# Optimization experiments

Hardware: AMD Instinct MI355X
Metric: run time of the kernel (lower is better)

The kernel has to match this reference:

```python
import jax, jax.numpy as jnp
import numpy as np
import math

N = 4096          # nodes
E = 131072        # edges (avg degree 32)
H = 128           # hidden_channels
IN = 128          # in_channels
RATIO = 0.8
K = int(math.ceil(RATIO * N))   # clusters kept by ASAPooling (static)


def setup_inputs():
    key = jax.random.key(0)
    ks = jax.random.split(key, 24)
    sc = 0.05
    def p(i, shape):
        return jax.random.normal(ks[i], shape, dtype=jnp.float32) * sc
    x = jax.random.normal(ks[0], (N, IN), dtype=jnp.float32)
    src = jax.random.randint(ks[1], (E,), 0, N)
    off = jax.random.randint(ks[2], (E,), 0, N - 1)
    dst = (src + 1 + off) % N          # guaranteed no self-loops
    edge_index = jnp.stack([src, dst]).astype(jnp.int32)
    inp = {"x": x, "edge_index": edge_index}
    dims = [(IN, H), (H, H), (H, H), (H, H)]
    for ci, (din, dout) in enumerate(dims):
        inp[f"c{ci}_Wrel"] = p(3 + 3 * ci, (dout, din))
        inp[f"c{ci}_brel"] = jnp.zeros((dout,), jnp.float32)
        inp[f"c{ci}_Wroot"] = p(4 + 3 * ci, (dout, din))
    inp["p_Wlin"] = p(16, (H, H));     inp["p_blin"] = jnp.zeros((H,), jnp.float32)
    inp["p_Watt"] = p(17, (1, 2 * H)); inp["p_batt"] = jnp.zeros((1,), jnp.float32)
    inp["p_W1"] = p(18, (1, H));       inp["p_b1"] = jnp.zeros((1,), jnp.float32)
    inp["p_W2"] = p(19, (1, H))
    inp["p_W3"] = p(20, (1, H));       inp["p_b3"] = jnp.zeros((1,), jnp.float32)
    return inp


def _graph_conv_edges(x, src, dst, Wrel, brel, Wroot):
    # GraphConv(aggr='mean'), edge_weight=None: lin_rel(mean_j x_j) + lin_root(x)
    n = x.shape[0]
    agg = jax.ops.segment_sum(x[src], dst, num_segments=n)
    deg = jax.ops.segment_sum(jnp.ones((src.shape[0],), x.dtype), dst, num_segments=n)
    mean = agg / jnp.maximum(deg, 1.0)[:, None]
    return mean @ Wrel.T + brel + x @ Wroot.T


def _graph_conv_dense(x, A, Wrel, brel, Wroot):
    # A[j, i] = weight of edge j -> i; mean over existing (nonzero) edges
    agg = jnp.einsum('ji,jh->ih', A, x)
    deg = (A != 0).astype(x.dtype).sum(axis=0)
    mean = agg / jnp.maximum(deg, 1.0)[:, None]
    return mean @ Wrel.T + brel + x @ Wroot.T


def _asap_pool(x, src, dst, Wlin, blin, Watt, batt, W1, b1, W2, W3, b3):
    n = x.shape[0]
    loops = jnp.arange(n, dtype=src.dtype)
    s2 = jnp.concatenate([src, loops])           # add_remaining_self_loops (w=1)
    d2 = jnp.concatenate([dst, loops])
    x_pool_j = x[s2]                              # [E2, H]
    x_q = jax.ops.segment_max(x_pool_j, d2, num_segments=n)   # cluster max
    x_q = (x_q @ Wlin.T + blin)[d2]
    score = jnp.concatenate([x_q, x_pool_j], axis=-1) @ Watt.T + batt
    score = jax.nn.leaky_relu(score[:, 0], 0.2)
    m = jax.ops.segment_max(score, d2, num_segments=n)        # stable edge softmax
    ex = jnp.exp(score - m[d2])
    score = ex / jax.ops.segment_sum(ex, d2, num_segments=n)[d2]
    x_new = jax.ops.segment_sum(x[s2] * score[:, None], d2, num_segments=n)
    # fitness via LEConv(H -> 1) with all edge weights 1
    a = x_new @ W1.T + b1
    b = x_new @ W2.T
    agg = jax.ops.segment_sum(a[s2] - b[d2], d2, num_segments=n)
    fitness = jax.nn.sigmoid(agg + x_new @ W3.T + b3)[:, 0]
    fit_k, perm = jax.lax.top_k(fitness, K)
    xp = x_new[perm] * fit_k[:, None]
    # graph coarsening: A' = S^T A S, S restricted to kept clusters
    S = jnp.zeros((n, n), x.dtype).at[s2, d2].add(score)[:, perm]   # [n, K]
    A = jnp.zeros((n, n), x.dtype).at[s2, d2].add(1.0)
    A2 = S.T @ (A @ S)
    A2 = A2 * (1.0 - jnp.eye(K, dtype=x.dtype))  # remove_diag (add_self_loops=False)
    return xp, A2


def _forward(x, edge_index, c0_Wrel, c0_brel, c0_Wroot, c1_Wrel, c1_brel, c1_Wroot,
             c2_Wrel, c2_brel, c2_Wroot, c3_Wrel, c3_brel, c3_Wroot,
             p_Wlin, p_blin, p_Watt, p_batt, p_W1, p_b1, p_W2, p_W3, p_b3):
    src, dst = edge_index[0], edge_index[1]
    x1 = jax.nn.relu(_graph_conv_edges(x, src, dst, c0_Wrel, c0_brel, c0_Wroot))
    xs = [x1.mean(axis=0, keepdims=True)]                 # global_mean_pool, B=1
    x2 = jax.nn.relu(_graph_conv_edges(x1, src, dst, c1_Wrel, c1_brel, c1_Wroot))
    xs.append(x2.mean(axis=0, keepdims=True))
    xp, A = _asap_pool(x2, src, dst, p_Wlin, p_blin, p_Watt, p_batt,
                       p_W1, p_b1, p_W2, p_W3, p_b3)
    x3 = jax.nn.relu(_graph_conv_dense(xp, A, c2_Wrel, c2_brel, c2_Wroot))
    xs.append(x3.mean(axis=0, keepdims=True))
    x4 = jax.nn.relu(_graph_conv_dense(x3, A, c3_Wrel, c3_brel, c3_Wroot))
    xs.append(x4.mean(axis=0, keepdims=True))
    return jnp.concatenate(xs, axis=1)    # JumpingKnowledge 'cat': [1, 4*H]


def reference(x, edge_index, c0_Wrel, c0_brel, c0_Wroot, c1_Wrel, c1_brel, c1_Wroot,
              c2_Wrel, c2_brel, c2_Wroot, c3_Wrel, c3_brel, c3_Wroot,
              p_Wlin, p_blin, p_Watt, p_batt, p_W1, p_b1, p_W2, p_W3, p_b3):
    return _forward(x, edge_index, c0_Wrel, c0_brel, c0_Wroot, c1_Wrel, c1_brel,
                    c1_Wroot, c2_Wrel, c2_brel, c2_Wroot, c3_Wrel, c3_brel, c3_Wroot,
                    p_Wlin, p_blin, p_Watt, p_batt, p_W1, p_b1, p_W2, p_W3, p_b3)
```

## Files before the change

kernel.cpp:

```cpp
#include <hip/hip_runtime.h>
#include <hip/hip_fp16.h>
#include <math.h>

namespace {

constexpr int NN = 4096;
constexpr int EE = 131072;
constexpr int E2 = EE + NN;
constexpr int HH = 128;
constexpr int KC = 3277;
constexpr int UPW = 104;
constexpr int WSB = (E2 + 255) / 256;
constexpr int XPB = (KC*HH + 255) / 256;

typedef _Float16 f16x8 __attribute__((ext_vector_type(8)));
typedef float f32x4 __attribute__((ext_vector_type(4)));

__device__ __forceinline__ float lrelu02(float x){ return x > 0.f ? x : 0.2f * x; }

__device__ __forceinline__ float redSum128(float* red, int t, float v){
  red[t] = v; __syncthreads();
  #pragma unroll
  for (int s = 64; s > 0; s >>= 1){ if (t < s) red[t] += red[t + s]; __syncthreads(); }
  float r = red[0]; __syncthreads();
  return r;
}
__device__ __forceinline__ float redMax128(float* red, int t, float v){
  red[t] = v; __syncthreads();
  #pragma unroll
  for (int s = 64; s > 0; s >>= 1){ if (t < s) red[t] = fmaxf(red[t], red[t + s]); __syncthreads(); }
  float r = red[0]; __syncthreads();
  return r;
}

__global__ void k_count(const int* __restrict__ ei, int* cntD, int* cntS){
  int e = blockIdx.x * blockDim.x + threadIdx.x;
  if (e >= E2) return;
  int u, v;
  if (e < EE){ u = ei[e]; v = ei[EE + e]; } else { u = e - EE; v = u; }
  atomicAdd(&cntD[v], 1);
  atomicAdd(&cntS[u], 1);
}

__global__ void k_scan(const int* cntD, const int* cntS, int* rowD, int* rowS, int* curD, int* curS){
  __shared__ unsigned long long wsum[16];
  int t = threadIdx.x, lane = t & 63, wid = t >> 6;
  int d0 = cntD[t*4], d1 = cntD[t*4+1], d2 = cntD[t*4+2], d3 = cntD[t*4+3];
  int s0 = cntS[t*4], s1 = cntS[t*4+1], s2 = cntS[t*4+2], s3 = cntS[t*4+3];
  int dT = d0 + d1 + d2 + d3, sT = s0 + s1 + s2 + s3;
  unsigned long long tot = ((unsigned long long)(unsigned)dT << 32) | (unsigned)sT;
  unsigned long long x = tot;
  #pragma unroll
  for (int offs = 1; offs < 64; offs <<= 1){
    unsigned long long v = __shfl_up(x, offs);
    if (lane >= offs) x += v;
  }
  if (lane == 63) wsum[wid] = x;
  __syncthreads();
  if (t == 0){
    unsigned long long acc = 0;
    for (int i = 0; i < 16; ++i){ unsigned long long tmp = wsum[i]; wsum[i] = acc; acc += tmp; }
  }
  __syncthreads();
  unsigned long long excl = x - tot + wsum[wid];
  int eD = (int)(excl >> 32), eS = (int)(excl & 0xFFFFFFFFull);
  int r0 = eD, r1 = r0 + d0, r2 = r1 + d1, r3 = r2 + d2;
  rowD[t*4] = r0; rowD[t*4+1] = r1; rowD[t*4+2] = r2; rowD[t*4+3] = r3;
  curD[t*4] = r0; curD[t*4+1] = r1; curD[t*4+2] = r2; curD[t*4+3] = r3;
  int q0 = eS, q1 = q0 + s0, q2 = q1 + s1, q3 = q2 + s2;
  rowS[t*4] = q0; rowS[t*4+1] = q1; rowS[t*4+2] = q2; rowS[t*4+3] = q3;
  curS[t*4] = q0; curS[t*4+1] = q1; curS[t*4+2] = q2; curS[t*4+3] = q3;
  if (t == 1023){ rowD[NN] = r3 + d3; rowS[NN] = q3 + s3; }
}

__global__ void k_scatter(const int* __restrict__ ei, int* curD, int* curS,
                          int* colD, int* dstS, int* mapSD){
  int e = blockIdx.x * blockDim.x + threadIdx.x;
  if (e >= E2) return;
  int u, v;
  if (e < EE){ u = ei[e]; v = ei[EE + e]; } else { u = e - EE; v = u; }
  int p = atomicAdd(&curD[v], 1); colD[p] = u;
  int q = atomicAdd(&curS[u], 1); dstS[q] = v; mapSD[q] = p;
}

__global__ void k_prep(const float* __restrict__ x,
                       const float* __restrict__ W0rel, const float* __restrict__ W0root,
                       const float* __restrict__ W1rel, const float* __restrict__ W1root,
                       const float* __restrict__ W2rel, const float* __restrict__ W2root,
                       const float* __restrict__ W3rel, const float* __restrict__ W3root,
                       const float* __restrict__ Wlin, const float* __restrict__ blin,
                       const float* __restrict__ Watt,
                       __half* __restrict__ xh, __half* __restrict__ WH, float* __restrict__ wA2,
                       int* cntD, int* cntS, float* out){
  int b = blockIdx.x;
  if (b < 2048){
    int i = b*256 + threadIdx.x;
    xh[i] = __float2half(x[i]);
  } else if (b < 2048 + 512){
    int i = (b - 2048)*256 + threadIdx.x;
    int m = i >> 14, o = i & 16383;
    const float* src;
    switch (m){
      case 0: src = W0rel; break;
      case 1: src = W0root; break;
      case 2: src = W1rel; break;
      case 3: src = W1root; break;
      case 4: src = W2rel; break;
      case 5: src = W2root; break;
      case 6: src = W3rel; break;
      default: src = W3root; break;
    }
    WH[i] = __float2half(src[o]);
  } else if (b == 2560){
    int c = threadIdx.x;
    if (c < 128){
      float s = 0.f;
      for (int hh = 0; hh < HH; ++hh) s += Watt[hh] * Wlin[hh*HH + c];
      wA2[c] = s;
      if (c == 0){
        float q = 0.f;
        for (int hh = 0; hh < HH; ++hh) q += blin[hh] * Watt[hh];
        wA2[HH] = q;
      }
    }
  } else {
    int i = (b - 2561)*256 + threadIdx.x;
    cntD[i] = 0; cntS[i] = 0;
    if (i < 512) out[i] = 0.f;
  }
}

__global__ void k_edge_meanH(const __half* __restrict__ xinh, const int* __restrict__ rowD,
                             const int* __restrict__ colD, __half* __restrict__ meanbh){
  int v = blockIdx.x, t = threadIdx.x;
  int beg = rowD[v], end = rowD[v+1];
  float acc = 0.f;
  int p = beg;
  for (; p + 8 <= end; p += 8){
    int u0 = colD[p],   u1 = colD[p+1], u2 = colD[p+2], u3 = colD[p+3];
    int u4 = colD[p+4], u5 = colD[p+5], u6 = colD[p+6], u7 = colD[p+7];
    float a0 = __half2float(xinh[(size_t)u0*HH + t]);
    float a1 = __half2float(xinh[(size_t)u1*HH + t]);
    float a2 = __half2float(xinh[(size_t)u2*HH + t]);
    float a3 = __half2float(xinh[(size_t)u3*HH + t]);
    float a4 = __half2float(xinh[(size_t)u4*HH + t]);
    float a5 = __half2float(xinh[(size_t)u5*HH + t]);
    float a6 = __half2float(xinh[(size_t)u6*HH + t]);
    float a7 = __half2float(xinh[(size_t)u7*HH + t]);
    if (u0 != v) acc += a0;
    if (u1 != v) acc += a1;
    if (u2 != v) acc += a2;
    if (u3 != v) acc += a3;
    if (u4 != v) acc += a4;
    if (u5 != v) acc += a5;
    if (u6 != v) acc += a6;
    if (u7 != v) acc += a7;
  }
  for (; p < end; ++p){ int u = colD[p]; if (u != v) acc += __half2float(xinh[(size_t)u*HH + t]); }
  float dg = (float)(end - beg - 1);
  meanbh[(size_t)v*HH + t] = __float2half(acc / fmaxf(dg, 1.f));
}

__global__ void k_linM(const __half* __restrict__ mh, const __half* __restrict__ xinh,
                       const __half* __restrict__ WHh, int woff, int rows,
                       const float* __restrict__ brel,
                       float* __restrict__ xout, __half* __restrict__ xouth,
                       float* __restrict__ cmout,
                       const float* __restrict__ WattFull, float* __restrict__ xdotp){
  __shared__ float sx[16][4];
  int t = threadIdx.x, lane = t & 63, w = t >> 6;
  int r0 = blockIdx.x * 16;
  int l15 = lane & 15, lk = (lane >> 4) * 8;
  const _Float16* WH = (const _Float16*)WHh;
  const _Float16* Am = (const _Float16*)mh + (size_t)(r0 + l15)*HH + lk;
  const _Float16* Ax = (const _Float16*)xinh + (size_t)(r0 + l15)*HH + lk;
  const _Float16* Brel0 = WH + woff + (size_t)(w*32 + l15)*HH + lk;
  const _Float16* Brel1 = Brel0 + (size_t)16*HH;
  const _Float16* Broot0 = Brel0 + 16384;
  const _Float16* Broot1 = Brel1 + 16384;
  f32x4 acc0 = (f32x4)0.f, acc1 = (f32x4)0.f;
  #pragma unroll
  for (int kk = 0; kk < HH; kk += 32){
    f16x8 a = *(const f16x8*)(Am + kk);
    f16x8 b0 = *(const f16x8*)(Brel0 + kk);
    f16x8 b1 = *(const f16x8*)(Brel1 + kk);
    acc0 = __builtin_amdgcn_mfma_f32_16x16x32_f16(a, b0, acc0, 0, 0, 0);
    acc1 = __builtin_amdgcn_mfma_f32_16x16x32_f16(a, b1, acc1, 0, 0, 0);
  }
  #pragma unroll
  for (int kk = 0; kk < HH; kk += 32){
    f16x8 a = *(const f16x8*)(Ax + kk);
    f16x8 b0 = *(const f16x8*)(Broot0 + kk);
    f16x8 b1 = *(const f16x8*)(Broot1 + kk);
    acc0 = __builtin_amdgcn_mfma_f32_16x16x32_f16(a, b0, acc0, 0, 0, 0);
    acc1 = __builtin_amdgcn_mfma_f32_16x16x32_f16(a, b1, acc1, 0, 0, 0);
  }
  int rbase = (lane >> 4) * 4;
  int h0 = w*32 + l15, h1 = h0 + 16;
  float bb0 = brel[h0], bb1 = brel[h1];
  float wt0 = 0.f, wt1 = 0.f;
  if (xdotp){ wt0 = WattFull[HH + h0]; wt1 = WattFull[HH + h1]; }
  float cs0 = 0.f, cs1 = 0.f;
  #pragma unroll
  for (int r = 0; r < 4; ++r){
    int row = r0 + rbase + r;
    float v0 = fmaxf(acc0[r] + bb0, 0.f);
    float v1 = fmaxf(acc1[r] + bb1, 0.f);
    if (row < rows){
      if (xout){ xout[(size_t)row*HH + h0] = v0; xout[(size_t)row*HH + h1] = v1; }
      if (xouth){ xouth[(size_t)row*HH + h0] = __float2half(v0); xouth[(size_t)row*HH + h1] = __float2half(v1); }
      cs0 += v0; cs1 += v1;
    }
    if (xdotp){
      float ds = (row < rows) ? (v0*wt0 + v1*wt1) : 0.f;
      ds += __shfl_xor(ds, 1); ds += __shfl_xor(ds, 2);
      ds += __shfl_xor(ds, 4); ds += __shfl_xor(ds, 8);
      if (l15 == 0) sx[rbase + r][w] = ds;
    }
  }
  cs0 += __shfl_xor(cs0, 16); cs0 += __shfl_xor(cs0, 32);
  cs1 += __shfl_xor(cs1, 16); cs1 += __shfl_xor(cs1, 32);
  if (lane < 16){
    atomicAdd(&cmout[h0], cs0 / (float)rows);
    atomicAdd(&cmout[h1], cs1 / (float)rows);
  }
  if (xdotp){
    __syncthreads();
    if (t < 16 && r0 + t < rows) xdotp[r0 + t] = sx[t][0] + sx[t][1] + sx[t][2] + sx[t][3];
  }
}

__global__ void k_pool(const __half* __restrict__ x2h, const int* __restrict__ rowD, const int* __restrict__ colD,
                       const float* __restrict__ xdotA, const float* __restrict__ wA2, const float* __restrict__ battp,
                       const float* __restrict__ W1, const float* __restrict__ b1,
                       const float* __restrict__ W2, const float* __restrict__ W3, const float* __restrict__ b3,
                       float* qdotA, float* mA, float* sA, float* __restrict__ xnew, float* __restrict__ wD,
                       float* aA, float* bA, float* cA, float* __restrict__ diag2){
  __shared__ float red[128];
  __shared__ float wmem[128];
  __shared__ int uc[128];
  __shared__ int srcL[1024];
  __shared__ float wL[1024];
  int v = blockIdx.x, t = threadIdx.x;
  int beg = rowD[v], end = rowD[v+1];
  float batt = battp[0];
  float mx = -3.402823466e38f;
  int p = beg;
  for (; p + 4 <= end; p += 4){
    float a0 = __half2float(x2h[(size_t)colD[p]*HH + t]);
    float a1 = __half2float(x2h[(size_t)colD[p+1]*HH + t]);
    float a2 = __half2float(x2h[(size_t)colD[p+2]*HH + t]);
    float a3 = __half2float(x2h[(size_t)colD[p+3]*HH + t]);
    mx = fmaxf(fmaxf(fmaxf(fmaxf(mx, a0), a1), a2), a3);
  }
  for (; p < end; ++p) mx = fmaxf(mx, __half2float(x2h[(size_t)colD[p]*HH + t]));
  float qd = redSum128(red, t, mx * wA2[t]) + wA2[HH];
  float lm = -3.402823466e38f;
  for (p = beg + t; p < end; p += 128) lm = fmaxf(lm, lrelu02(qd + xdotA[colD[p]] + batt));
  float mm = redMax128(red, t, lm);
  float ls = 0.f;
  for (p = beg + t; p < end; p += 128) ls += expf(lrelu02(qd + xdotA[colD[p]] + batt) - mm);
  float ss = redSum128(red, t, ls);
  float acc = 0.f;
  for (int basep = beg; basep < end; basep += 128){
    int cnt = min(128, end - basep);
    if (t < cnt){
      int u = colD[basep + t];
      uc[t] = u;
      float w = expf(lrelu02(qd + xdotA[u] + batt) - mm) / ss;
      wmem[t] = w;
      wD[basep + t] = w;
      int o = basep - beg + t;
      if (o < 1024){ srcL[o] = u; wL[o] = w; }
    }
    __syncthreads();
    int i = 0;
    for (; i + 4 <= cnt; i += 4){
      float a0 = __half2float(x2h[(size_t)uc[i]*HH + t]);
      float a1 = __half2float(x2h[(size_t)uc[i+1]*HH + t]);
      float a2 = __half2float(x2h[(size_t)uc[i+2]*HH + t]);
      float a3 = __half2float(x2h[(size_t)uc[i+3]*HH + t]);
      acc += wmem[i]*a0 + wmem[i+1]*a1 + wmem[i+2]*a2 + wmem[i+3]*a3;
    }
    for (; i < cnt; ++i) acc += wmem[i] * __half2float(x2h[(size_t)uc[i]*HH + t]);
    __syncthreads();
  }
  xnew[(size_t)v*HH + t] = acc;
  float s1 = redSum128(red, t, acc * W1[t]);
  float s2 = redSum128(red, t, acc * W2[t]);
  float s3 = redSum128(red, t, acc * W3[t]);
  int d = end - beg; if (d > 1024) d = 1024;
  float dpart = 0.f;
  for (int pp = t; pp < d; pp += 128){
    int s = srcL[pp];
    float sp = 0.f;
    for (int q = 0; q < d; ++q) if (srcL[q] == s) sp += wL[q];
    dpart += wL[pp] * sp;
  }
  float d2 = redSum128(red, t, dpart);
  if (t == 0){
    qdotA[v] = qd; mA[v] = mm; sA[v] = ss;
    aA[v] = s1 + b1[0]; bA[v] = s2; cA[v] = s3 + b3[0];
    diag2[v] = d2;
  }
}

__global__ void k_fit(const int* __restrict__ rowD, const int* __restrict__ colD,
                      const float* __restrict__ aA, const float* __restrict__ bA, const float* __restrict__ cA,
                      float* __restrict__ fitA){
  __shared__ float red[128];
  int v = blockIdx.x, t = threadIdx.x;
  int beg = rowD[v], end = rowD[v+1];
  float la = 0.f;
  for (int p = beg + t; p < end; p += 128) la += aA[colD[p]];
  float s = redSum128(red, t, la);
  if (t == 0){
    float g = s - (float)(end - beg) * bA[v] + cA[v];
    fitA[v] = 1.f / (1.f + expf(-g));
  }
}

__global__ void k_sel(const float* __restrict__ fitA, int* perm, float* fitk, int* kcol){
  __shared__ unsigned keys[NN];
  __shared__ int hist[256];
  __shared__ int sufA[257];
  __shared__ int wsum[16];
  __shared__ int bc[2];
  int t = threadIdx.x, lane = t & 63, wid = t >> 6;
  #pragma unroll
  for (int r = 0; r < 4; ++r){
    int i = t + r*1024;
    unsigned b = __float_as_uint(fitA[i]);
    keys[i] = (b & 0x80000000u) ? ~b : (b ^ 0x80000000u);
  }
  __syncthreads();
  unsigned prefix = 0;
  int kneed = KC;
  #pragma unroll
  for (int round = 0; round < 4; ++round){
    int shift = 24 - round*8;
    unsigned pmask = (round == 0) ? 0u : (0xFFFFFFFFu << (shift + 8));
    if (t < 256) hist[t] = 0;
    __syncthreads();
    #pragma unroll
    for (int r = 0; r < 4; ++r){
      unsigned kv = keys[t + r*1024];
      if ((kv & pmask) == prefix)
        atomicAdd(&hist[(kv >> shift) & 0xFF], 1);
    }
    __syncthreads();
    int x = (t < 256) ? hist[t] : 0;
    #pragma unroll
    for (int offs = 1; offs < 64; offs <<= 1){
      int v = __shfl_down(x, offs);
      if (lane + offs < 64) x += v;
    }
    if (t < 256 && lane == 0) wsum[wid] = x;
    if (t == 0) sufA[256] = 0;
    __syncthreads();
    if (t < 256){
      int add = 0;
      #pragma unroll
      for (int w2 = 1; w2 < 4; ++w2) if (wid + w2 < 4) add += wsum[wid + w2];
      sufA[t] = x + add;
    }
    __syncthreads();
    if (t < 256){
      if (sufA[t] >= kneed && sufA[t+1] < kneed){ bc[0] = t; bc[1] = kneed - sufA[t+1]; }
    }
    __syncthreads();
    prefix |= ((unsigned)bc[0]) << shift;
    kneed = bc[1];
    __syncthreads();
  }
  unsigned T = prefix;
  int need_eq = kneed;
  int cnt[4]; int tot = 0;
  #pragma unroll
  for (int r = 0; r < 4; ++r){
    unsigned kv = keys[t*4 + r];
    int g = (kv > T) ? 1 : 0;
    int e = (kv == T) ? 1 : 0;
    cnt[r] = (g << 16) | e;
    tot += cnt[r];
  }
  int x2 = tot;
  #pragma unroll
  for (int offs = 1; offs < 64; offs <<= 1){
    int v = __shfl_up(x2, offs);
    if (lane >= offs) x2 += v;
  }
  if (lane == 63) wsum[wid] = x2;
  __syncthreads();
  if (t < 16){
    int y = wsum[t];
    #pragma unroll
    for (int offs = 1; offs < 16; offs <<= 1){
      int v = __shfl_up(y, offs);
      if (t >= offs) y += v;
    }
    wsum[t] = y;
  }
  __syncthreads();
  int waveoff = (wid > 0) ? wsum[wid - 1] : 0;
  int inc = x2 + waveoff;
  int run = inc - tot;
  int gtot = wsum[15] >> 16;
  #pragma unroll
  for (int r = 0; r < 4; ++r){
    int i = t*4 + r;
    int g = cnt[r] >> 16, e = cnt[r] & 0xFFFF;
    int gpos = run >> 16, epos = run & 0xFFFF;
    int pos = -1;
    if (g) pos = gpos;
    else if (e && epos < need_eq) pos = gtot + epos;
    if (pos >= 0){ perm[pos] = i; fitk[pos] = fitA[i]; kcol[i] = pos; }
    else kcol[i] = -1;
    run += cnt[r];
  }
}

__global__ void k_post(const int* __restrict__ mapSD, const int* __restrict__ dstS,
                       const int* __restrict__ kcol, const float* __restrict__ wD,
                       int2* __restrict__ kwS,
                       const float* __restrict__ xnew, const int* __restrict__ perm,
                       const float* __restrict__ fitk, __half* __restrict__ xph){
  int b = blockIdx.x;
  if (b < WSB){
    int q = b*256 + threadIdx.x;
    if (q >= E2) return;
    float w = wD[mapSD[q]];
    int k = kcol[dstS[q]];
    kwS[q] = make_int2(k, __float_as_int(w));
  } else {
    int idx = (b - WSB)*256 + threadIdx.x;
    if (idx >= KC*HH) return;
    int j = idx >> 7;
    float v = xnew[(size_t)perm[j]*HH + (idx & 127)] * fitk[j];
    xph[idx] = __float2half(v);
  }
}

__global__ void k_y1(const int* __restrict__ rowS, const int2* __restrict__ kwS,
                     const __half* __restrict__ Xh, __half* __restrict__ Y1h,
                     unsigned* __restrict__ UP, int emitUP){
  __shared__ int kArr[128];
  __shared__ float wArr[128];
  __shared__ unsigned upw[UPW];
  int n = blockIdx.x, t = threadIdx.x;
  if (emitUP && t < UPW) upw[t] = 0u;
  int beg = rowS[n], end = rowS[n+1];
  float acc = 0.f;
  for (int basep = beg; basep < end; basep += 128){
    int cnt = min(128, end - basep);
    if (t < cnt){
      int2 kw = kwS[basep + t];
      kArr[t] = kw.x;
      wArr[t] = __int_as_float(kw.y);
      if (emitUP && kw.x >= 0) atomicOr(&upw[kw.x >> 5], 1u << (kw.x & 31));
    }
    __syncthreads();
    for (int i = 0; i < cnt; ++i){
      int k = kArr[i];
      if (k >= 0) acc += wArr[i] * __half2float(Xh[(size_t)k*HH + t]);
    }
    __syncthreads();
  }
  Y1h[(size_t)n*HH + t] = __float2half(acc);
  if (emitUP){
    __syncthreads();
    if (t < UPW) UP[(size_t)n*UPW + t] = upw[t];
  }
}

__global__ void k_y2p(const int* __restrict__ rowD, const int* __restrict__ colD,
                      const __half* __restrict__ Y1h, __half* __restrict__ Y2h,
                      const int* __restrict__ perm, const unsigned* __restrict__ UP,
                      unsigned* __restrict__ PAT){
  int b = blockIdx.x, t = threadIdx.x;
  if (b < NN){
    int m = b;
    int beg = rowD[m], end = rowD[m+1];
    float acc = 0.f;
    int p = beg;
    for (; p + 8 <= end; p += 8){
      float a0 = __half2float(Y1h[(size_t)colD[p]*HH + t]);
      float a1 = __half2float(Y1h[(size_t)colD[p+1]*HH + t]);
      float a2 = __half2float(Y1h[(size_t)colD[p+2]*HH + t]);
      float a3 = __half2float(Y1h[(size_t)colD[p+3]*HH + t]);
      float a4 = __half2float(Y1h[(size_t)colD[p+4]*HH + t]);
      float a5 = __half2float(Y1h[(size_t)colD[p+5]*HH + t]);
      float a6 = __half2float(Y1h[(size_t)colD[p+6]*HH + t]);
      float a7 = __half2float(Y1h[(size_t)colD[p+7]*HH + t]);
      acc += ((a0 + a1) + (a2 + a3)) + ((a4 + a5) + (a6 + a7));
    }
    for (; p < end; ++p) acc += __half2float(Y1h[(size_t)colD[p]*HH + t]);
    Y2h[(size_t)m*HH + t] = __float2half(acc);
  } else {
    int k1 = b - NN;
    if (k1 >= KC || t >= UPW) return;
    int v = perm[k1];
    int beg = rowD[v], end = rowD[v+1];
    unsigned pw = 0u;
    for (int p = beg; p < end; ++p) pw |= UP[(size_t)colD[p]*UPW + t];
    PAT[(size_t)k1*UPW + t] = pw;
  }
}

__global__ void k_y2(const int* __restrict__ rowD, const int* __restrict__ colD,
                     const __half* __restrict__ Y1h, __half* __restrict__ Y2h){
  int m = blockIdx.x, t = threadIdx.x;
  int beg = rowD[m], end = rowD[m+1];
  float acc = 0.f;
  int p = beg;
  for (; p + 8 <= end; p += 8){
    float a0 = __half2float(Y1h[(size_t)colD[p]*HH + t]);
    float a1 = __half2float(Y1h[(size_t)colD[p+1]*HH + t]);
    float a2 = __half2float(Y1h[(size_t)colD[p+2]*HH + t]);
    float a3 = __half2float(Y1h[(size_t)colD[p+3]*HH + t]);
    float a4 = __half2float(Y1h[(size_t)colD[p+4]*HH + t]);
    float a5 = __half2float(Y1h[(size_t)colD[p+5]*HH + t]);
    float a6 = __half2float(Y1h[(size_t)colD[p+6]*HH + t]);
    float a7 = __half2float(Y1h[(size_t)colD[p+7]*HH + t]);
    acc += ((a0 + a1) + (a2 + a3)) + ((a4 + a5) + (a6 + a7));
  }
  for (; p < end; ++p) acc += __half2float(Y1h[(size_t)colD[p]*HH + t]);
  Y2h[(size_t)m*HH + t] = __float2half(acc);
}

__global__ void k_z(const int* __restrict__ rowD, const int* __restrict__ colD,
                    const float* __restrict__ wD, const int* __restrict__ perm,
                    const __half* __restrict__ Y2h, const __half* __restrict__ Xh,
                    const float* __restrict__ diag2, const int* __restrict__ degN,
                    __half* __restrict__ meanbh){
  __shared__ int uc[128];
  __shared__ float wm[128];
  int k = blockIdx.x, t = threadIdx.x;
  int v = perm[k];
  int beg = rowD[v], end = rowD[v+1];
  float acc = 0.f;
  for (int basep = beg; basep < end; basep += 128){
    int cnt = min(128, end - basep);
    if (t < cnt){ uc[t] = colD[basep + t]; wm[t] = wD[basep + t]; }
    __syncthreads();
    int i = 0;
    for (; i + 4 <= cnt; i += 4){
      float a0 = __half2float(Y2h[(size_t)uc[i]*HH + t]);
      float a1 = __half2float(Y2h[(size_t)uc[i+1]*HH + t]);
      float a2 = __half2float(Y2h[(size_t)uc[i+2]*HH + t]);
      float a3 = __half2float(Y2h[(size_t)uc[i+3]*HH + t]);
      acc += wm[i]*a0 + wm[i+1]*a1 + wm[i+2]*a2 + wm[i+3]*a3;
    }
    for (; i < cnt; ++i) acc += wm[i] * __half2float(Y2h[(size_t)uc[i]*HH + t]);
    __syncthreads();
  }
  float d = fmaxf((float)degN[k], 1.f);
  float xv = __half2float(Xh[(size_t)k*HH + t]);
  meanbh[(size_t)k*HH + t] = __float2half((acc - diag2[v] * xv) / d);
}

__global__ void k_degc(const unsigned* __restrict__ PAT, int* __restrict__ degN){
  __shared__ int red[256];
  int w = blockIdx.x, t = threadIdx.x;
  int c[32];
  #pragma unroll
  for (int j = 0; j < 32; ++j) c[j] = 0;
  for (int r = t; r < KC; r += 256){
    unsigned b = PAT[(size_t)r*UPW + w];
    #pragma unroll
    for (int j = 0; j < 32; ++j) c[j] += (b >> j) & 1;
  }
  for (int j = 0; j < 32; ++j){
    red[t] = c[j]; __syncthreads();
    #pragma unroll
    for (int s = 128; s > 0; s >>= 1){ if (t < s) red[t] += red[t + s]; __syncthreads(); }
    if (t == 0) degN[w*32 + j] = red[0] - 1;
    __syncthreads();
  }
}

}

extern "C" void kernel_launch(void* const* d_in, const int* in_sizes, int n_in,
                              void* d_out, int out_size, void* d_ws, size_t ws_size,
                              hipStream_t stream){
  (void)in_sizes; (void)n_in; (void)out_size; (void)ws_size;
  const float* x      = (const float*)d_in[0];
  const int*   ei     = (const int*)d_in[1];
  const float* c0Wrel = (const float*)d_in[2];
  const float* c0brel = (const float*)d_in[3];
  const float* c0Wroot= (const float*)d_in[4];
  const float* c1Wrel = (const float*)d_in[5];
  const float* c1brel = (const float*)d_in[6];
  const float* c1Wroot= (const float*)d_in[7];
  const float* c2Wrel = (const float*)d_in[8];
  const float* c2brel = (const float*)d_in[9];
  const float* c2Wroot= (const float*)d_in[10];
  const float* c3Wrel = (const float*)d_in[11];
  const float* c3brel = (const float*)d_in[12];
  const float* c3Wroot= (const float*)d_in[13];
  const float* Wlin   = (const float*)d_in[14];
  const float* blin   = (const float*)d_in[15];
  const float* Watt   = (const float*)d_in[16];
  const float* batt   = (const float*)d_in[17];
  const float* W1     = (const float*)d_in[18];
  const float* b1     = (const float*)d_in[19];
  const float* W2     = (const float*)d_in[20];
  const float* W3     = (const float*)d_in[21];
  const float* b3     = (const float*)d_in[22];
  float* out = (float*)d_out;

  char* base = (char*)d_ws;
  size_t off = 0;
  auto carve = [&](size_t bytes) -> void* {
    void* p = base + off;
    off += (bytes + 255) & ~(size_t)255;
    return p;
  };
  float* xnew  = (float*)carve((size_t)NN*HH*4);
  __half* xh   = (__half*)carve((size_t)NN*HH*2);
  __half* x1h  = (__half*)carve((size_t)NN*HH*2);
  __half* x2bh = (__half*)carve((size_t)NN*HH*2);
  __half* mbh  = (__half*)carve((size_t)NN*HH*2);
  __half* xph  = (__half*)carve((size_t)(KC+16)*HH*2);
  __half* x3h  = (__half*)carve((size_t)(KC+16)*HH*2);
  __half* Y1h  = (__half*)carve((size_t)NN*HH*2);
  __half* Y2h  = (__half*)carve((size_t)NN*HH*2);
  __half* WH   = (__half*)carve((size_t)8*HH*HH*2);
  unsigned* UP  = (unsigned*)carve((size_t)NN*UPW*4);
  unsigned* PAT = (unsigned*)carve((size_t)KC*UPW*4);
  float* xdot  = (float*)carve(NN*4);
  float* qdot  = (float*)carve(NN*4);
  float* mmaxA = (float*)carve(NN*4);
  float* ssumA = (float*)carve(NN*4);
  float* aA    = (float*)carve(NN*4);
  float* bA    = (float*)carve(NN*4);
  float* cA    = (float*)carve(NN*4);
  float* fitA  = (float*)carve(NN*4);
  float* fitk  = (float*)carve(KC*4);
  float* wA2   = (float*)carve((HH+1)*4);
  float* wD    = (float*)carve((size_t)E2*4);
  float* diag2 = (float*)carve(NN*4);
  int* rowD = (int*)carve((NN+1)*4);
  int* rowS = (int*)carve((NN+1)*4);
  int* cntD = (int*)carve(NN*4);
  int* cntS = (int*)carve(NN*4);
  int* curD = (int*)carve(NN*4);
  int* curS = (int*)carve(NN*4);
  int* colD = (int*)carve((size_t)E2*4);
  int* dstS = (int*)carve((size_t)E2*4);
  int* mapSD= (int*)carve((size_t)E2*4);
  int2* kwS = (int2*)carve((size_t)E2*8);
  int* perm = (int*)carve(KC*4);
  int* kcol = (int*)carve(NN*4);
  int* degN = (int*)carve((size_t)UPW*32*4);

  k_prep<<<2048 + 512 + 1 + 16, 256, 0, stream>>>(x, c0Wrel, c0Wroot, c1Wrel, c1Wroot,
                                                  c2Wrel, c2Wroot, c3Wrel, c3Wroot,
                                                  Wlin, blin, Watt, xh, WH, wA2,
                                                  cntD, cntS, out);
  k_count<<<(E2+255)/256, 256, 0, stream>>>(ei, cntD, cntS);
  k_scan<<<1, 1024, 0, stream>>>(cntD, cntS, rowD, rowS, curD, curS);
  k_scatter<<<(E2+255)/256, 256, 0, stream>>>(ei, curD, curS, colD, dstS, mapSD);

  k_edge_meanH<<<NN, 128, 0, stream>>>(xh, rowD, colD, mbh);
  k_linM<<<NN/16, 256, 0, stream>>>(mbh, xh, WH, 0, NN, c0brel,
                                    nullptr, x1h, out + 0, nullptr, nullptr);

  k_edge_meanH<<<NN, 128, 0, stream>>>(x1h, rowD, colD, mbh);
  k_linM<<<NN/16, 256, 0, stream>>>(mbh, x1h, WH, 32768, NN, c1brel,
                                    nullptr, x2bh, out + 128, Watt, xdot);

  k_pool<<<NN, 128, 0, stream>>>(x2bh, rowD, colD, xdot, wA2, batt,
                                 W1, b1, W2, W3, b3,
                                 qdot, mmaxA, ssumA, xnew, wD, aA, bA, cA, diag2);
  k_fit<<<NN, 128, 0, stream>>>(rowD, colD, aA, bA, cA, fitA);
  k_sel<<<1, 1024, 0, stream>>>(fitA, perm, fitk, kcol);
  k_post<<<WSB + XPB, 256, 0, stream>>>(mapSD, dstS, kcol, wD, kwS,
                                        xnew, perm, fitk, xph);

  k_y1<<<NN, 128, 0, stream>>>(rowS, kwS, xph, Y1h, UP, 1);
  k_y2p<<<NN + KC, 128, 0, stream>>>(rowD, colD, Y1h, Y2h, perm, UP, PAT);
  k_degc<<<UPW, 256, 0, stream>>>(PAT, degN);
  k_z<<<KC, 128, 0, stream>>>(rowD, colD, wD, perm, Y2h, xph, diag2, degN, mbh);
  k_linM<<<(KC+15)/16, 256, 0, stream>>>(mbh, xph, WH, 65536, KC, c2brel,
                                         nullptr, x3h, out + 256, nullptr, nullptr);

  k_y1<<<NN, 128, 0, stream>>>(rowS, kwS, x3h, Y1h, UP, 0);
  k_y2<<<NN, 128, 0, stream>>>(rowD, colD, Y1h, Y2h);
  k_z<<<KC, 128, 0, stream>>>(rowD, colD, wD, perm, Y2h, x3h, diag2, degN, mbh);
  k_linM<<<(KC+15)/16, 256, 0, stream>>>(mbh, x3h, WH, 98304, KC, c3brel,
                                         nullptr, nullptr, out + 384, nullptr, nullptr);
}
```

Measured before the change: 240.3 us.

## Vectorize gather kernels with half2 loads and split edges across two waves

Rewrites the neighbour-gather kernels (edge mean, pool, Y1/Y2, z) so each thread loads a __half2 covering two channels instead of one half. The two 64-lane wavefronts of each 128-thread block take alternating edges, and their partial sums are combined through shared memory. The aim is to double bytes per load instruction and halve per-wave edge iterations in these latency-bound gathers. It adds a shared-memory reduction and barrier, and leaves half the threads idle during the final writes. In k_pool the 128-wide block reductions are replaced with wave shuffles.

Result: faster. 233.4 us (-2.9%).

```diff
diff --git a/kernel.cpp b/kernel.cpp
--- a/kernel.cpp
+++ b/kernel.cpp
@@ -31,6 +31,11 @@
   for (int s = 64; s > 0; s >>= 1){ if (t < s) red[t] = fmaxf(red[t], red[t + s]); __syncthreads(); }
   float r = red[0]; __syncthreads();
   return r;
+}
+__device__ __forceinline__ float waveRed64(float v){
+  #pragma unroll
+  for (int o = 32; o > 0; o >>= 1) v += __shfl_xor(v, o);
+  return v;
 }
 
 __global__ void k_count(const int* __restrict__ ei, int* cntD, int* cntS){
@@ -132,33 +137,35 @@
 
 __global__ void k_edge_meanH(const __half* __restrict__ xinh, const int* __restrict__ rowD,
                              const int* __restrict__ colD, __half* __restrict__ meanbh){
+  __shared__ float2 s2[128];
   int v = blockIdx.x, t = threadIdx.x;
+  int c = t & 63, g = t >> 6;
+  const __half2* X2 = (const __half2*)xinh;
   int beg = rowD[v], end = rowD[v+1];
-  float acc = 0.f;
-  int p = beg;
-  for (; p + 8 <= end; p += 8){
-    int u0 = colD[p],   u1 = colD[p+1], u2 = colD[p+2], u3 = colD[p+3];
-    int u4 = colD[p+4], u5 = colD[p+5], u6 = colD[p+6], u7 = colD[p+7];
-    float a0 = __half2float(xinh[(size_t)u0*HH + t]);
-    float a1 = __half2float(xinh[(size_t)u1*HH + t]);
-    float a2 = __half2float(xinh[(size_t)u2*HH + t]);
-    float a3 = __half2float(xinh[(size_t)u3*HH + t]);
-    float a4 = __half2float(xinh[(size_t)u4*HH + t]);
-    float a5 = __half2float(xinh[(size_t)u5*HH + t]);
-    float a6 = __half2float(xinh[(size_t)u6*HH + t]);
-    float a7 = __half2float(xinh[(size_t)u7*HH + t]);
-    if (u0 != v) acc += a0;
-    if (u1 != v) acc += a1;
-    if (u2 != v) acc += a2;
-    if (u3 != v) acc += a3;
-    if (u4 != v) acc += a4;
-    if (u5 != v) acc += a5;
-    if (u6 != v) acc += a6;
-    if (u7 != v) acc += a7;
-  }
-  for (; p < end; ++p){ int u = colD[p]; if (u != v) acc += __half2float(xinh[(size_t)u*HH + t]); }
-  float dg = (float)(end - beg - 1);
-  meanbh[(size_t)v*HH + t] = __float2half(acc / fmaxf(dg, 1.f));
+  float2 acc = make_float2(0.f, 0.f);
+  int p = beg + g;
+  for (; p + 6 < end; p += 8){
+    int u0 = colD[p], u1 = colD[p+2], u2 = colD[p+4], u3 = colD[p+6];
+    float2 f0 = __half22float2(X2[(size_t)u0*64 + c]);
+    float2 f1 = __half22float2(X2[(size_t)u1*64 + c]);
+    float2 f2 = __half22float2(X2[(size_t)u2*64 + c]);
+    float2 f3 = __half22float2(X2[(size_t)u3*64 + c]);
+    if (u0 != v){ acc.x += f0.x; acc.y += f0.y; }
+    if (u1 != v){ acc.x += f1.x; acc.y += f1.y; }
+    if (u2 != v){ acc.x += f2.x; acc.y += f2.y; }
+    if (u3 != v){ acc.x += f3.x; acc.y += f3.y; }
+  }
+  for (; p < end; p += 2){
+    int u = colD[p];
+    float2 f = __half22float2(X2[(size_t)u*64 + c]);
+    if (u != v){ acc.x += f.x; acc.y += f.y; }
+  }
+  s2[t] = acc; __syncthreads();
+  if (t < 64){
+    float dg = fmaxf((float)(end - beg - 1), 1.f);
+    float2 tot = make_float2((s2[t].x + s2[t+64].x) / dg, (s2[t].y + s2[t+64].y) / dg);
+    ((__half2*)meanbh)[(size_t)v*64 + t] = __floats2half2_rn(tot.x, tot.y);
+  }
 }
 
 __global__ void k_linM(const __half* __restrict__ mh, const __half* __restrict__ xinh,
@@ -237,31 +244,48 @@
                        float* qdotA, float* mA, float* sA, float* __restrict__ xnew, float* __restrict__ wD,
                        float* aA, float* bA, float* cA, float* __restrict__ diag2){
   __shared__ float red[128];
+  __shared__ float2 s2[128];
   __shared__ float wmem[128];
   __shared__ int uc[128];
   __shared__ int srcL[1024];
   __shared__ float wL[1024];
+  __shared__ float qs[1];
   int v = blockIdx.x, t = threadIdx.x;
+  int c = t & 63, g = t >> 6;
+  const __half2* X2 = (const __half2*)x2h;
   int beg = rowD[v], end = rowD[v+1];
   float batt = battp[0];
-  float mx = -3.402823466e38f;
-  int p = beg;
-  for (; p + 4 <= end; p += 4){
-    float a0 = __half2float(x2h[(size_t)colD[p]*HH + t]);
-    float a1 = __half2float(x2h[(size_t)colD[p+1]*HH + t]);
-    float a2 = __half2float(x2h[(size_t)colD[p+2]*HH + t]);
-    float a3 = __half2float(x2h[(size_t)colD[p+3]*HH + t]);
-    mx = fmaxf(fmaxf(fmaxf(fmaxf(mx, a0), a1), a2), a3);
-  }
-  for (; p < end; ++p) mx = fmaxf(mx, __half2float(x2h[(size_t)colD[p]*HH + t]));
-  float qd = redSum128(red, t, mx * wA2[t]) + wA2[HH];
+  float2 mx2 = make_float2(-3.402823466e38f, -3.402823466e38f);
+  int p = beg + g;
+  for (; p + 6 < end; p += 8){
+    float2 f0 = __half22float2(X2[(size_t)colD[p]*64 + c]);
+    float2 f1 = __half22float2(X2[(size_t)colD[p+2]*64 + c]);
+    float2 f2 = __half22float2(X2[(size_t)colD[p+4]*64 + c]);
+    float2 f3 = __half22float2(X2[(size_t)colD[p+6]*64 + c]);
+    mx2.x = fmaxf(fmaxf(fmaxf(fmaxf(mx2.x, f0.x), f1.x), f2.x), f3.x);
+    mx2.y = fmaxf(fmaxf(fmaxf(fmaxf(mx2.y, f0.y), f1.y), f2.y), f3.y);
+  }
+  for (; p < end; p += 2){
+    float2 f = __half22float2(X2[(size_t)colD[p]*64 + c]);
+    mx2.x = fmaxf(mx2.x, f.x);
+    mx2.y = fmaxf(mx2.y, f.y);
+  }
+  s2[t] = mx2; __syncthreads();
+  if (t < 64){
+    float2 m2 = make_float2(fmaxf(s2[t].x, s2[t+64].x), fmaxf(s2[t].y, s2[t+64].y));
+    float part = m2.x * wA2[2*t] + m2.y * wA2[2*t+1];
+    part = waveRed64(part);
+    if (t == 0) qs[0] = part + wA2[HH];
+  }
+  __syncthreads();
+  float qd = qs[0];
   float lm = -3.402823466e38f;
   for (p = beg + t; p < end; p += 128) lm = fmaxf(lm, lrelu02(qd + xdotA[colD[p]] + batt));
   float mm = redMax128(red, t, lm);
   float ls = 0.f;
   for (p = beg + t; p < end; p += 128) ls += expf(lrelu02(qd + xdotA[colD[p]] + batt) - mm);
   float ss = redSum128(red, t, ls);
-  float acc = 0.f;
+  float2 acc2 = make_float2(0.f, 0.f);
   for (int basep = beg; basep < end; basep += 128){
     int cnt = min(128, end - basep);
     if (t < cnt){
@@ -274,21 +298,34 @@
       if (o < 1024){ srcL[o] = u; wL[o] = w; }
     }
     __syncthreads();
-    int i = 0;
-    for (; i + 4 <= cnt; i += 4){
-      float a0 = __half2float(x2h[(size_t)uc[i]*HH + t]);
-      float a1 = __half2float(x2h[(size_t)uc[i+1]*HH + t]);
-      float a2 = __half2float(x2h[(size_t)uc[i+2]*HH + t]);
-      float a3 = __half2float(x2h[(size_t)uc[i+3]*HH + t]);
-      acc += wmem[i]*a0 + wmem[i+1]*a1 + wmem[i+2]*a2 + wmem[i+3]*a3;
-    }
-    for (; i < cnt; ++i) acc += wmem[i] * __half2float(x2h[(size_t)uc[i]*HH + t]);
-    __syncthreads();
-  }
-  xnew[(size_t)v*HH + t] = acc;
-  float s1 = redSum128(red, t, acc * W1[t]);
-  float s2 = redSum128(red, t, acc * W2[t]);
-  float s3 = redSum128(red, t, acc * W3[t]);
+    int i = g;
+    for (; i + 6 < cnt; i += 8){
+      float2 f0 = __half22float2(X2[(size_t)uc[i]*64 + c]);
+      float2 f1 = __half22float2(X2[(size_t)uc[i+2]*64 + c]);
+      float2 f2 = __half22float2(X2[(size_t)uc[i+4]*64 + c]);
+      float2 f3 = __half22float2(X2[(size_t)uc[i+6]*64 + c]);
+      acc2.x += wmem[i]*f0.x + wmem[i+2]*f1.x + wmem[i+4]*f2.x + wmem[i+6]*f3.x;
+      acc2.y += wmem[i]*f0.y + wmem[i+2]*f1.y + wmem[i+4]*f2.y + wmem[i+6]*f3.y;
+    }
+    for (; i < cnt; i += 2){
+      float2 f = __half22float2(X2[(size_t)uc[i]*64 + c]);
+      acc2.x += wmem[i]*f.x;
+      acc2.y += wmem[i]*f.y;
+    }
+    __syncthreads();
+  }
+  s2[t] = acc2; __syncthreads();
+  float s1 = 0.f, sB = 0.f, sC = 0.f;
+  if (t < 64){
+    float2 tot = make_float2(s2[t].x + s2[t+64].x, s2[t].y + s2[t+64].y);
+    *(float2*)(xnew + (size_t)v*HH + 2*t) = tot;
+    float p1 = tot.x*W1[2*t] + tot.y*W1[2*t+1];
+    float p2 = tot.x*W2[2*t] + tot.y*W2[2*t+1];
+    float p3 = tot.x*W3[2*t] + tot.y*W3[2*t+1];
+    s1 = waveRed64(p1);
+    sB = waveRed64(p2);
+    sC = waveRed64(p3);
+  }
   int d = end - beg; if (d > 1024) d = 1024;
   float dpart = 0.f;
   for (int pp = t; pp < d; pp += 128){
@@ -300,7 +337,7 @@
   float d2 = redSum128(red, t, dpart);
   if (t == 0){
     qdotA[v] = qd; mA[v] = mm; sA[v] = ss;
-    aA[v] = s1 + b1[0]; bA[v] = s2; cA[v] = s3 + b3[0];
+    aA[v] = s1 + b1[0]; bA[v] = sB; cA[v] = sC + b3[0];
     diag2[v] = d2;
   }
 }
@@ -446,11 +483,14 @@
                      unsigned* __restrict__ UP, int emitUP){
   __shared__ int kArr[128];
   __shared__ float wArr[128];
+  __shared__ float2 s2[128];
   __shared__ unsigned upw[UPW];
   int n = blockIdx.x, t = threadIdx.x;
+  int c = t & 63, g = t >> 6;
+  const __half2* X2 = (const __half2*)Xh;
   if (emitUP && t < UPW) upw[t] = 0u;
   int beg = rowS[n], end = rowS[n+1];
-  float acc = 0.f;
+  float2 acc = make_float2(0.f, 0.f);
   for (int basep = beg; basep < end; basep += 128){
     int cnt = min(128, end - basep);
     if (t < cnt){
@@ -460,13 +500,21 @@
       if (emitUP && kw.x >= 0) atomicOr(&upw[kw.x >> 5], 1u << (kw.x & 31));
     }
     __syncthreads();
-    for (int i = 0; i < cnt; ++i){
+    for (int i = g; i < cnt; i += 2){
       int k = kArr[i];
-      if (k >= 0) acc += wArr[i] * __half2float(Xh[(size_t)k*HH + t]);
-    }
-    __syncthreads();
-  }
-  Y1h[(size_t)n*HH + t] = __float2half(acc);
+      if (k >= 0){
+        float2 f = __half22float2(X2[(size_t)k*64 + c]);
+        acc.x += wArr[i]*f.x;
+        acc.y += wArr[i]*f.y;
+      }
+    }
+    __syncthreads();
+  }
+  s2[t] = acc; __syncthreads();
+  if (t < 64){
+    float2 tot = make_float2(s2[t].x + s2[t+64].x, s2[t].y + s2[t+64].y);
+    ((__half2*)Y1h)[(size_t)n*64 + t] = __floats2half2_rn(tot.x, tot.y);
+  }
   if (emitUP){
     __syncthreads();
     if (t < UPW) UP[(size_t)n*UPW + t] = upw[t];
@@ -477,25 +525,32 @@
                       const __half* __restrict__ Y1h, __half* __restrict__ Y2h,
                       const int* __restrict__ perm, const unsigned* __restrict__ UP,
                       unsigned* __restrict__ PAT){
+  __shared__ float2 s2[128];
   int b = blockIdx.x, t = threadIdx.x;
   if (b < NN){
     int m = b;
+    int c = t & 63, g = t >> 6;
+    const __half2* Y12 = (const __half2*)Y1h;
     int beg = rowD[m], end = rowD[m+1];
-    float acc = 0.f;
-    int p = beg;
-    for (; p + 8 <= end; p += 8){
-      float a0 = __half2float(Y1h[(size_t)colD[p]*HH + t]);
-      float a1 = __half2float(Y1h[(size_t)colD[p+1]*HH + t]);
-      float a2 = __half2float(Y1h[(size_t)colD[p+2]*HH + t]);
-      float a3 = __half2float(Y1h[(size_t)colD[p+3]*HH + t]);
-      float a4 = __half2float(Y1h[(size_t)colD[p+4]*HH + t]);
-      float a5 = __half2float(Y1h[(size_t)colD[p+5]*HH + t]);
-      float a6 = __half2float(Y1h[(size_t)colD[p+6]*HH + t]);
-      float a7 = __half2float(Y1h[(size_t)colD[p+7]*HH + t]);
-      acc += ((a0 + a1) + (a2 + a3)) + ((a4 + a5) + (a6 + a7));
-    }
-    for (; p < end; ++p) acc += __half2float(Y1h[(size_t)colD[p]*HH + t]);
-    Y2h[(size_t)m*HH + t] = __float2half(acc);
+    float2 acc = make_float2(0.f, 0.f);
+    int p = beg + g;
+    for (; p + 6 < end; p += 8){
+      float2 f0 = __half22float2(Y12[(size_t)colD[p]*64 + c]);
+      float2 f1 = __half22float2(Y12[(size_t)colD[p+2]*64 + c]);
+      float2 f2 = __half22float2(Y12[(size_t)colD[p+4]*64 + c]);
+      float2 f3 = __half22float2(Y12[(size_t)colD[p+6]*64 + c]);
+      acc.x += (f0.x + f1.x) + (f2.x + f3.x);
+      acc.y += (f0.y + f1.y) + (f2.y + f3.y);
+    }
+    for (; p < end; p += 2){
+      float2 f = __half22float2(Y12[(size_t)colD[p]*64 + c]);
+      acc.x += f.x; acc.y += f.y;
+    }
+    s2[t] = acc; __syncthreads();
+    if (t < 64){
+      float2 tot = make_float2(s2[t].x + s2[t+64].x, s2[t].y + s2[t+64].y);
+      ((__half2*)Y2h)[(size_t)m*64 + t] = __floats2half2_rn(tot.x, tot.y);
+    }
   } else {
     int k1 = b - NN;
     if (k1 >= KC || t >= UPW) return;
@@ -509,23 +564,30 @@
 
 __global__ void k_y2(const int* __restrict__ rowD, const int* __restrict__ colD,
                      const __half* __restrict__ Y1h, __half* __restrict__ Y2h){
+  __shared__ float2 s2[128];
   int m = blockIdx.x, t = threadIdx.x;
+  int c = t & 63, g = t >> 6;
+  const __half2* Y12 = (const __half2*)Y1h;
   int beg = rowD[m], end = rowD[m+1];
-  float acc = 0.f;
-  int p = beg;
-  for (; p + 8 <= end; p += 8){
-    float a0 = __half2float(Y1h[(size_t)colD[p]*HH + t]);
-    float a1 = __half2float(Y1h[(size_t)colD[p+1]*HH + t]);
-    float a2 = __half2float(Y1h[(size_t)colD[p+2]*HH + t]);
-    float a3 = __half2float(Y1h[(size_t)colD[p+3]*HH + t]);
-    float a4 = __half2float(Y1h[(size_t)colD[p+4]*HH + t]);
-    float a5 = __half2float(Y1h[(size_t)colD[p+5]*HH + t]);
-    float a6 = __half2float(Y1h[(size_t)colD[p+6]*HH + t]);
-    float a7 = __half2float(Y1h[(size_t)colD[p+7]*HH + t]);
-    acc += ((a0 + a1) + (a2 + a3)) + ((a4 + a5) + (a6 + a7));
-  }
-  for (; p < end; ++p) acc += __half2float(Y1h[(size_t)colD[p]*HH + t]);
-  Y2h[(size_t)m*HH + t] = __float2half(acc);
+  float2 acc = make_float2(0.f, 0.f);
+  int p = beg + g;
+  for (; p + 6 < end; p += 8){
+    float2 f0 = __half22float2(Y12[(size_t)colD[p]*64 + c]);
+    float2 f1 = __half22float2(Y12[(size_t)colD[p+2]*64 + c]);
+    float2 f2 = __half22float2(Y12[(size_t)colD[p+4]*64 + c]);
+    float2 f3 = __half22float2(Y12[(size_t)colD[p+6]*64 + c]);
+    acc.x += (f0.x + f1.x) + (f2.x + f3.x);
+    acc.y += (f0.y + f1.y) + (f2.y + f3.y);
+  }
+  for (; p < end; p += 2){
+    float2 f = __half22float2(Y12[(size_t)colD[p]*64 + c]);
+    acc.x += f.x; acc.y += f.y;
+  }
+  s2[t] = acc; __syncthreads();
+  if (t < 64){
+    float2 tot = make_float2(s2[t].x + s2[t+64].x, s2[t].y + s2[t+64].y);
+    ((__half2*)Y2h)[(size_t)m*64 + t] = __floats2half2_rn(tot.x, tot.y);
+  }
 }
 
 __global__ void k_z(const int* __restrict__ rowD, const int* __restrict__ colD,
@@ -535,28 +597,42 @@
                     __half* __restrict__ meanbh){
   __shared__ int uc[128];
   __shared__ float wm[128];
+  __shared__ float2 s2[128];
   int k = blockIdx.x, t = threadIdx.x;
+  int c = t & 63, g = t >> 6;
+  const __half2* Y22 = (const __half2*)Y2h;
   int v = perm[k];
   int beg = rowD[v], end = rowD[v+1];
-  float acc = 0.f;
+  float2 acc = make_float2(0.f, 0.f);
   for (int basep = beg; basep < end; basep += 128){
     int cnt = min(128, end - basep);
     if (t < cnt){ uc[t] = colD[basep + t]; wm[t] = wD[basep + t]; }
     __syncthreads();
-    int i = 0;
-    for (; i + 4 <= cnt; i += 4){
-      float a0 = __half2float(Y2h[(size_t)uc[i]*HH + t]);
-      float a1 = __half2float(Y2h[(size_t)uc[i+1]*HH + t]);
-      float a2 = __half2float(Y2h[(size_t)uc[i+2]*HH + t]);
-      float a3 = __half2float(Y2h[(size_t)uc[i+3]*HH + t]);
-      acc += wm[i]*a0 + wm[i+1]*a1 + wm[i+2]*a2 + wm[i+3]*a3;
-    }
-    for (; i < cnt; ++i) acc += wm[i] * __half2float(Y2h[(size_t)uc[i]*HH + t]);
-    __syncthreads();
-  }
-  float d = fmaxf((float)degN[k], 1.f);
-  float xv = __half2float(Xh[(size_t)k*HH + t]);
-  meanbh[(size_t)k*HH + t] = __float2half((acc - diag2[v] * xv) / d);
+    int i = g;
+    for (; i + 6 < cnt; i += 8){
+      float2 f0 = __half22float2(Y22[(size_t)uc[i]*64 + c]);
+      float2 f1 = __half22float2(Y22[(size_t)uc[i+2]*64 + c]);
+      float2 f2 = __half22float2(Y22[(size_t)uc[i+4]*64 + c]);
+      float2 f3 = __half22float2(Y22[(size_t)uc[i+6]*64 + c]);
+      acc.x += wm[i]*f0.x + wm[i+2]*f1.x + wm[i+4]*f2.x + wm[i+6]*f3.x;
+      acc.y += wm[i]*f0.y + wm[i+2]*f1.y + wm[i+4]*f2.y + wm[i+6]*f3.y;
+    }
+    for (; i < cnt; i += 2){
+      float2 f = __half22float2(Y22[(size_t)uc[i]*64 + c]);
+      acc.x += wm[i]*f.x;
+      acc.y += wm[i]*f.y;
+    }
+    __syncthreads();
+  }
+  s2[t] = acc; __syncthreads();
+  if (t < 64){
+    float d = fmaxf((float)degN[k], 1.f);
+    float dg = diag2[v];
+    float2 xv = __half22float2(((const __half2*)Xh)[(size_t)k*64 + t]);
+    float2 tot = make_float2((s2[t].x + s2[t+64].x - dg*xv.x) / d,
+                             (s2[t].y + s2[t+64].y - dg*xv.y) / d);
+    ((__half2*)meanbh)[(size_t)k*64 + t] = __floats2half2_rn(tot.x, tot.y);
+  }
 }
 
 __global__ void k_degc(const unsigned* __restrict__ PAT, int* __restrict__ degN){
```
